# Performance work log

Hardware: AMD Instinct MI355X
Metric: run time of the kernel (lower is better)

## Reference

```python
import jax, jax.numpy as jnp
import numpy as np

EPS = 1e-6
NUM_SPECIAL = 4
NUM_HEADS = 16


def _rms_norm(x, w, eps=EPS):
    # x: [..., d], normalize over last dim
    var = jnp.mean(jnp.square(x), axis=-1, keepdims=True)
    return x * jax.lax.rsqrt(var + eps) * w


def _rotate_half(x):
    d = x.shape[-1] // 2
    return jnp.concatenate([-x[..., d:], x[..., :d]], axis=-1)


def _apply_rotary(q, k, cos, sin):
    # q,k: [B,H,N,hd]; cos,sin: [N,hd] -> broadcast [1,1,N,hd]
    cos = cos[None, None, :, :]
    sin = sin[None, None, :, :]
    q_out = q * cos + _rotate_half(q) * sin
    k_out = k * cos + _rotate_half(k) * sin
    return q_out, k_out


def _make_2d_mask(seq_len, num_special, window):
    # special tokens attend / are attended fully; patches use 2D local box
    patch_len = seq_len - num_special
    gs = int(round(patch_len ** 0.5))
    idx = jnp.arange(seq_len)
    special = idx < num_special
    p = idx - num_special
    row = p // gs
    col = p % gs
    special_case = special[:, None] | special[None, :]
    swa = (jnp.abs(row[:, None] - row[None, :]) <= window) & (
        jnp.abs(col[:, None] - col[None, :]) <= window)
    return special_case | swa  # [N, N] bool


def setup_inputs() -> dict:
    key = jax.random.key(0)
    ks = jax.random.split(key, 7)
    B, N, C = 4, 1028, 1024
    hd = C // NUM_HEADS
    return {
        "hidden_states": jax.random.normal(ks[0], (B, N, C), dtype=jnp.float32),
        "cos": jax.random.uniform(ks[1], (N, hd), dtype=jnp.float32),
        "sin": jax.random.uniform(ks[2], (N, hd), dtype=jnp.float32),
        "qkv_w": jax.random.normal(ks[3], (3 * C, C), dtype=jnp.float32) * (C ** -0.5),
        "out_w": jax.random.normal(ks[4], (C, C), dtype=jnp.float32) * (C ** -0.5),
        "norm_q_w": jnp.ones((hd,), dtype=jnp.float32),
        "norm_k_w": jnp.ones((hd,), dtype=jnp.float32),
        "sliding_window": 2,
    }


def reference(hidden_states, cos, sin, qkv_w, out_w, norm_q_w, norm_k_w, sliding_window):
    B, N, C = hidden_states.shape
    H = NUM_HEADS
    hd = C // H

    # fused QKV projection (nn.Linear: x @ W^T)
    qkv = jnp.einsum('bnc,dc->bnd', hidden_states, qkv_w)
    qkv = qkv.reshape(B, N, 3, H, hd).transpose(2, 0, 3, 1, 4)  # [3,B,H,N,hd]
    q, k, v = qkv[0], qkv[1], qkv[2]

    # per-head-dim RMSNorm on q and k
    q = _rms_norm(q, norm_q_w)
    k = _rms_norm(k, norm_k_w)

    # RoPE
    q, k = _apply_rotary(q, k, cos, sin)

    # 2D sliding-window + special-token mask
    mask = _make_2d_mask(N, NUM_SPECIAL, sliding_window)  # [N,N]

    scale = 1.0 / jnp.sqrt(jnp.asarray(hd, dtype=q.dtype))
    scores = jnp.einsum('bhqd,bhkd->bhqk', q, k) * scale
    neg = jnp.asarray(jnp.finfo(scores.dtype).min, dtype=scores.dtype)
    scores = jnp.where(mask[None, None, :, :], scores, neg)
    probs = jax.nn.softmax(scores, axis=-1)
    attn = jnp.einsum('bhqk,bhkd->bhqd', probs, v)  # [B,H,N,hd]

    attn = attn.transpose(0, 2, 1, 3).reshape(B, N, C)
    return jnp.einsum('bnc,dc->bnd', attn, out_w)
```

## Files before the change

kernel.cpp:

```cpp
#include <hip/hip_runtime.h>
#include <hip/hip_bf16.h>
#include <stdint.h>

typedef __bf16 bf16;
typedef __attribute__((ext_vector_type(8))) __bf16 bf16x8;
typedef __attribute__((ext_vector_type(4))) __bf16 bf16x4;
typedef __attribute__((ext_vector_type(4))) float f32x4;

#define NSEQ 1028
#define CDIM 1024
#define NHEADS 16
#define HD 64
#define BHN 64
#define NPAD 1088
#define M_REAL 4112
#define MTILES 33

static __device__ __forceinline__ void async_copy16(bf16* lds, const bf16* g) {
  __builtin_amdgcn_global_load_lds(
      (const __attribute__((address_space(1))) uint32_t*)g,
      (__attribute__((address_space(3))) uint32_t*)lds, 16, 0, 0);
}

__global__ __launch_bounds__(256) void cast_pad_kernel(const float* __restrict__ src,
                                                       bf16* __restrict__ dst,
                                                       long n_src, long n_dst) {
  long t = (long)blockIdx.x * 256 + threadIdx.x;
  long stride = (long)gridDim.x * 256;
  for (long j = t * 4; j < n_dst; j += stride * 4) {
    bf16x4 o;
    if (j + 4 <= n_src) {
      float4 v = *(const float4*)(src + j);
      o[0] = (bf16)v.x; o[1] = (bf16)v.y; o[2] = (bf16)v.z; o[3] = (bf16)v.w;
    } else {
      for (int k = 0; k < 4; k++) o[k] = (bf16)((j + k < n_src) ? src[j + k] : 0.0f);
    }
    *(bf16x4*)(dst + j) = o;
  }
}

template <int EPI, int NSTRIP>
__global__ __launch_bounds__(256) void gemm_bf16_kernel(
    const bf16* __restrict__ A, const bf16* __restrict__ Bm,
    bf16* __restrict__ q_bf, bf16* __restrict__ k_bf, bf16* __restrict__ v_raw,
    float* __restrict__ outF,
    const float* __restrict__ cosb, const float* __restrict__ sinb,
    const float* __restrict__ nqw, const float* __restrict__ nkw) {
  constexpr int K = CDIM;
  constexpr int N = NSTRIP * 8 * 128;
  __shared__ __attribute__((aligned(16))) bf16 As[2][128 * 64];
  __shared__ __attribute__((aligned(16))) bf16 Bs[2][128 * 64];
  const int tid = threadIdx.x;
  const int lane = tid & 63;
  const int wid = tid >> 6;
  const int wr = wid >> 1, wc = wid & 1;
  const int l15 = lane & 15, l4 = lane >> 4;

  const int xcd = blockIdx.x & 7;
  const int pos = blockIdx.x >> 3;
  const int nloc = pos % NSTRIP;
  const int mi = pos / NSTRIP;
  const int n0 = (xcd * NSTRIP + nloc) << 7;
  const int m0 = (mi < MTILES - 1) ? (mi << 7) : (M_REAL - 128);

  f32x4 acc[4][4] = {};

  size_t a_base[4], b_base[4];
#pragma unroll
  for (int s = 0; s < 4; s++) {
    int c = tid + s * 256;
    int row = c >> 3, ch = c & 7;
    int chs = ch ^ (row & 7);
    a_base[s] = (size_t)(m0 + row) * K + (chs << 3);
    b_base[s] = (size_t)(n0 + row) * K + (chs << 3);
  }

#define STAGE(bufi, ktof)                                         \
  {                                                               \
    _Pragma("unroll")                                             \
    for (int s = 0; s < 4; s++) {                                 \
      int c = tid + s * 256;                                      \
      async_copy16(&As[bufi][c * 8], A + a_base[s] + (ktof));     \
      async_copy16(&Bs[bufi][c * 8], Bm + b_base[s] + (ktof));    \
    }                                                             \
  }

  const int nt = K >> 6;
  STAGE(0, 0);

  for (int t = 0; t < nt; ++t) {
    if (t + 1 < nt) {
      STAGE((t + 1) & 1, (t + 1) << 6);
      asm volatile("s_waitcnt vmcnt(8)" ::: "memory");
    } else {
      asm volatile("s_waitcnt vmcnt(0)" ::: "memory");
    }
    __builtin_amdgcn_s_barrier();

    const int rsw = l15 & 7;
    const int cur = t & 1;
    bf16x8 af[2][4], bfr[2][4];
#pragma unroll
    for (int h = 0; h < 2; h++)
#pragma unroll
      for (int i = 0; i < 4; i++)
        af[h][i] = *(const bf16x8*)&As[cur][(wr * 64 + i * 16 + l15) * 64 +
                                            (((h * 4 + l4) ^ rsw) << 3)];
#pragma unroll
    for (int h = 0; h < 2; h++)
#pragma unroll
      for (int j = 0; j < 4; j++)
        bfr[h][j] = *(const bf16x8*)&Bs[cur][(wc * 64 + j * 16 + l15) * 64 +
                                             (((h * 4 + l4) ^ rsw) << 3)];

#pragma unroll
    for (int h = 0; h < 2; h++)
#pragma unroll
      for (int i = 0; i < 4; i++)
#pragma unroll
        for (int j = 0; j < 4; j++)
          acc[i][j] = __builtin_amdgcn_mfma_f32_16x16x32_bf16(af[h][i], bfr[h][j], acc[i][j], 0, 0, 0);

    asm volatile("s_waitcnt lgkmcnt(0)" ::: "memory");
    __builtin_amdgcn_s_barrier();
  }
#undef STAGE

  if (EPI == 0) {
    const int d_base = n0 + wc * 64;
    const int tsel = d_base >> 10;
    const int hh = (d_base & 1023) >> 6;
    if (tsel == 2) {
#pragma unroll
      for (int i = 0; i < 4; i++)
#pragma unroll
        for (int r = 0; r < 4; r++) {
          int m = m0 + wr * 64 + i * 16 + l4 * 4 + r;
          int b = m / NSEQ, n = m % NSEQ;
          size_t rb = ((size_t)(b * NHEADS + hh) * NSEQ + n) * HD;
#pragma unroll
          for (int j = 0; j < 4; j++)
            v_raw[rb + j * 16 + l15] = (bf16)acc[i][j][r];
        }
    } else {
      const float* wn = (tsel == 0) ? nqw : nkw;
      bf16* dst = (tsel == 0) ? q_bf : k_bf;
      float wv[4];
#pragma unroll
      for (int j = 0; j < 4; j++) wv[j] = wn[j * 16 + l15];
#pragma unroll
      for (int i = 0; i < 4; i++)
#pragma unroll
        for (int r = 0; r < 4; r++) {
          int m = m0 + wr * 64 + i * 16 + l4 * 4 + r;
          float ss = 0.0f;
#pragma unroll
          for (int j = 0; j < 4; j++) { float x = acc[i][j][r]; ss += x * x; }
          ss += __shfl_xor(ss, 1);
          ss += __shfl_xor(ss, 2);
          ss += __shfl_xor(ss, 4);
          ss += __shfl_xor(ss, 8);
          float rms = rsqrtf(ss * (1.0f / HD) + 1e-6f);
          int b = m / NSEQ, n = m % NSEQ;
          float qn[4];
#pragma unroll
          for (int j = 0; j < 4; j++) qn[j] = acc[i][j][r] * rms * wv[j];
          size_t rb = ((size_t)(b * NHEADS + hh) * NPAD + n) * HD;
#pragma unroll
          for (int j = 0; j < 4; j++) {
            float c = cosb[n * HD + j * 16 + l15];
            float s = sinb[n * HD + j * 16 + l15];
            float rot = (j < 2) ? -qn[j + 2] : qn[j - 2];
            dst[rb + j * 16 + l15] = (bf16)(qn[j] * c + rot * s);
          }
        }
    }
  } else {
#pragma unroll
    for (int i = 0; i < 4; i++)
#pragma unroll
      for (int j = 0; j < 4; j++) {
        int d = n0 + wc * 64 + j * 16 + l15;
        int mrow = m0 + wr * 64 + i * 16 + l4 * 4;
#pragma unroll
        for (int r = 0; r < 4; r++) {
          int m = mrow + r;
          outF[(size_t)m * N + d] = acc[i][j][r];
        }
      }
  }
}

__global__ __launch_bounds__(256) void v_transpose_kernel(const bf16* __restrict__ v_raw,
                                                          bf16* __restrict__ vT) {
  __shared__ bf16 tile[64][65];
  int bh = blockIdx.y, c = blockIdx.x;
  int tid = threadIdx.x;
#pragma unroll
  for (int jj = 0; jj < 16; jj++) {
    int idx = tid + jj * 256;
    int i = idx >> 6, e = idx & 63;
    int n = (c == 0) ? i : (64 * c - 60 + i);
    bool ok = (c == 0) ? (i < 4) : (n < NSEQ);
    tile[i][e] = ok ? v_raw[((size_t)bh * NSEQ + n) * HD + e] : (bf16)0.0f;
  }
  __syncthreads();
#pragma unroll
  for (int jj = 0; jj < 16; jj++) {
    int idx = tid + jj * 256;
    int e = idx >> 6, i = idx & 63;
    vT[((size_t)bh * HD + e) * NPAD + 64 * c + i] = tile[i][e];
  }
}

__global__ __launch_bounds__(256) void attn_kernel(
    const bf16* __restrict__ Q, const bf16* __restrict__ Kb, const bf16* __restrict__ Vt,
    bf16* __restrict__ att, const int* __restrict__ winp) {
  __shared__ __attribute__((aligned(16))) bf16 P_s[4][16][72];
  __shared__ float o_s[4][4][64];
  __shared__ float ml_s[4][2][16];
  const int bh = blockIdx.y, qt = blockIdx.x;
  const int W = winp[0];
  const int tid = threadIdx.x, w = tid >> 6, lane = tid & 63;
  const int l15 = lane & 15, l4 = lane >> 4;
  const size_t qkbase = (size_t)bh * NPAD * HD;
  const size_t vtb = (size_t)bh * HD * NPAD;
  const bool is_spec = (qt == 16);

  const int qrow0 = is_spec ? 0 : (4 + qt * 64 + w * 16);
  bf16x8 aq0 = *(const bf16x8*)&Q[qkbase + (size_t)(qrow0 + l15) * HD + l4 * 8];
  bf16x8 aq1 = *(const bf16x8*)&Q[qkbase + (size_t)(qrow0 + l15) * HD + 32 + l4 * 8];

  float mrow[4], lrow[4];
  f32x4 o[4] = {};
#pragma unroll
  for (int r = 0; r < 4; r++) { mrow[r] = -1e30f; lrow[r] = 0.0f; }

  int p0, pstep, pmax, toff;
  if (is_spec) {
    p0 = w; pstep = 4; pmax = 16; toff = -1;
  } else {
    int ta = ((2 * qt - W + 64) >> 1) - 32;
    int tb = (2 * qt + 1 + W) >> 1;
    ta = ta < 0 ? 0 : ta;
    tb = tb > 15 ? 15 : tb;
    p0 = 0; pstep = 1; pmax = tb - ta + 1; toff = ta - 1;
  }

  for (int p = p0; p <= pmax; p += pstep) {
    const bool sp = (p == 0);
    const int tau = toff + p;
    const int krow0 = sp ? 0 : (4 + tau * 64);
    const int vcol0 = sp ? 0 : (64 + tau * 64);

    f32x4 sacc[4] = {};
#pragma unroll
    for (int kf = 0; kf < 4; kf++) {
      const bf16* kp = &Kb[qkbase + (size_t)(krow0 + kf * 16 + l15) * HD];
      bf16x8 b0 = *(const bf16x8*)(kp + l4 * 8);
      bf16x8 b1 = *(const bf16x8*)(kp + 32 + l4 * 8);
      sacc[kf] = __builtin_amdgcn_mfma_f32_16x16x32_bf16(aq0, b0, sacc[kf], 0, 0, 0);
      sacc[kf] = __builtin_amdgcn_mfma_f32_16x16x32_bf16(aq1, b1, sacc[kf], 0, 0, 0);
    }

    float pvv[4][4];
#pragma unroll
    for (int kf = 0; kf < 4; kf++)
#pragma unroll
      for (int r = 0; r < 4; r++) {
        float s = sacc[kf][r] * 0.125f;
        bool valid;
        if (sp) {
          valid = (kf == 0) && (l15 < 4);
        } else if (is_spec) {
          valid = true;
        } else {
          int p_k = tau * 64 + kf * 16 + l15;
          int p_q = qt * 64 + w * 16 + l4 * 4 + r;
          int dr = (p_q >> 5) - (p_k >> 5); dr = dr < 0 ? -dr : dr;
          int dc = (p_q & 31) - (p_k & 31); dc = dc < 0 ? -dc : dc;
          valid = (dr <= W) && (dc <= W);
        }
        pvv[kf][r] = valid ? s : -1e30f;
      }

#pragma unroll
    for (int r = 0; r < 4; r++) {
      float mx = fmaxf(fmaxf(pvv[0][r], pvv[1][r]), fmaxf(pvv[2][r], pvv[3][r]));
#pragma unroll
      for (int mm = 1; mm < 16; mm <<= 1) mx = fmaxf(mx, __shfl_xor(mx, mm));
      float mnew = fmaxf(mrow[r], mx);
      float scale = __expf(mrow[r] - mnew);
      float rs = 0.0f;
#pragma unroll
      for (int kf = 0; kf < 4; kf++) {
        float pp = __expf(pvv[kf][r] - mnew);
        pvv[kf][r] = pp;
        rs += pp;
      }
#pragma unroll
      for (int mm = 1; mm < 16; mm <<= 1) rs += __shfl_xor(rs, mm);
      lrow[r] = lrow[r] * scale + rs;
      mrow[r] = mnew;
#pragma unroll
      for (int f = 0; f < 4; f++) o[f][r] *= scale;
    }

#pragma unroll
    for (int kf = 0; kf < 4; kf++)
#pragma unroll
      for (int r = 0; r < 4; r++)
        P_s[w][l4 * 4 + r][kf * 16 + l15] = (bf16)pvv[kf][r];

    bf16x8 pa0 = *(const bf16x8*)&P_s[w][l15][l4 * 8];
    bf16x8 pa1 = *(const bf16x8*)&P_s[w][l15][32 + l4 * 8];
#pragma unroll
    for (int f = 0; f < 4; f++) {
      const bf16* vp = &Vt[vtb + (size_t)(f * 16 + l15) * NPAD + vcol0];
      bf16x8 v0 = *(const bf16x8*)(vp + l4 * 8);
      bf16x8 v1 = *(const bf16x8*)(vp + 32 + l4 * 8);
      o[f] = __builtin_amdgcn_mfma_f32_16x16x32_bf16(pa0, v0, o[f], 0, 0, 0);
      o[f] = __builtin_amdgcn_mfma_f32_16x16x32_bf16(pa1, v1, o[f], 0, 0, 0);
    }
  }

  const int b = bh >> 4, h = bh & 15;
  if (!is_spec) {
#pragma unroll
    for (int f = 0; f < 4; f++)
#pragma unroll
      for (int r = 0; r < 4; r++) {
        int n = qrow0 + l4 * 4 + r;
        att[((size_t)(b * NSEQ + n)) * CDIM + h * HD + f * 16 + l15] =
            (bf16)(o[f][r] / lrow[r]);
      }
  } else {
    if (l4 == 0) {
#pragma unroll
      for (int f = 0; f < 4; f++)
#pragma unroll
        for (int r = 0; r < 4; r++) o_s[w][r][f * 16 + l15] = o[f][r];
      if (l15 == 0)
#pragma unroll
        for (int r = 0; r < 4; r++) { ml_s[w][0][r] = mrow[r]; ml_s[w][1][r] = lrow[r]; }
    }
    __syncthreads();
    int row = tid >> 6, dim = tid & 63;
    float M = -1e30f;
#pragma unroll
    for (int ww = 0; ww < 4; ww++) M = fmaxf(M, ml_s[ww][0][row]);
    float L = 0.0f, val = 0.0f;
#pragma unroll
    for (int ww = 0; ww < 4; ww++) {
      float e = __expf(ml_s[ww][0][row] - M);
      L += e * ml_s[ww][1][row];
      val += e * o_s[ww][row][dim];
    }
    att[((size_t)(b * NSEQ + row)) * CDIM + h * HD + dim] = (bf16)(val / L);
  }
}

extern "C" void kernel_launch(void* const* d_in, const int* in_sizes, int n_in,
                              void* d_out, int out_size, void* d_ws, size_t ws_size,
                              hipStream_t stream) {
  const float* hidden = (const float*)d_in[0];
  const float* cosb = (const float*)d_in[1];
  const float* sinb = (const float*)d_in[2];
  const float* qkv_w = (const float*)d_in[3];
  const float* out_w = (const float*)d_in[4];
  const float* norm_q_w = (const float*)d_in[5];
  const float* norm_k_w = (const float*)d_in[6];
  const int* win = (const int*)d_in[7];
  float* out = (float*)d_out;

  char* ws = (char*)d_ws;
  size_t off = 0;
  auto alloc = [&](size_t bytes) {
    char* p = ws + off;
    off += (bytes + 255) & ~(size_t)255;
    return p;
  };
  bf16* A_bf  = (bf16*)alloc((size_t)M_REAL * CDIM * 2);
  bf16* W1    = (bf16*)alloc((size_t)3 * CDIM * CDIM * 2);
  bf16* W2    = (bf16*)alloc((size_t)CDIM * CDIM * 2);
  bf16* v_raw = (bf16*)alloc((size_t)BHN * NSEQ * HD * 2);
  bf16* q_bf  = (bf16*)alloc((size_t)BHN * NPAD * HD * 2);
  bf16* k_bf  = (bf16*)alloc((size_t)BHN * NPAD * HD * 2);
  bf16* vT    = (bf16*)alloc((size_t)BHN * HD * NPAD * 2);
  bf16* att   = (bf16*)alloc((size_t)M_REAL * CDIM * 2);
  (void)ws_size; (void)in_sizes; (void)n_in; (void)out_size;

  cast_pad_kernel<<<2048, 256, 0, stream>>>(hidden, A_bf, (long)M_REAL * CDIM, (long)M_REAL * CDIM);
  cast_pad_kernel<<<1024, 256, 0, stream>>>(qkv_w, W1, (long)3 * CDIM * CDIM, (long)3 * CDIM * CDIM);
  cast_pad_kernel<<<512, 256, 0, stream>>>(out_w, W2, (long)CDIM * CDIM, (long)CDIM * CDIM);

  gemm_bf16_kernel<0, 3><<<792, 256, 0, stream>>>(
      A_bf, W1, q_bf, k_bf, v_raw, nullptr, cosb, sinb, norm_q_w, norm_k_w);
  v_transpose_kernel<<<dim3(17, 64), 256, 0, stream>>>(v_raw, vT);
  attn_kernel<<<dim3(17, 64), 256, 0, stream>>>(q_bf, k_bf, vT, att, win);
  gemm_bf16_kernel<1, 1><<<264, 256, 0, stream>>>(
      att, W2, nullptr, nullptr, nullptr, out, nullptr, nullptr, nullptr, nullptr);
}
```

Baseline: 136.8 us.

## Fuse three cast launches and halve GEMM K-tile for higher occupancy

Merges the three fp32-to-bf16 cast kernels into one launch that walks a concatenated index space, removing two kernel launches and their tail effects. The GEMM K-step shrinks from 64 to 32, which halves LDS per block (to 32 KB). A new swizzle scheme fits the 4-chunk rows, and launch_bounds now requests 4 blocks per CU for more occupancy. The cost is twice as many barrier-synchronized iterations, with less MFMA work per barrier to hide global-load latency.

```diff
diff --git a/kernel.cpp b/kernel.cpp
--- a/kernel.cpp
+++ b/kernel.cpp
@@ -22,25 +22,27 @@
       (__attribute__((address_space(3))) uint32_t*)lds, 16, 0, 0);
 }
 
-__global__ __launch_bounds__(256) void cast_pad_kernel(const float* __restrict__ src,
-                                                       bf16* __restrict__ dst,
-                                                       long n_src, long n_dst) {
+__global__ __launch_bounds__(256) void cast3_kernel(
+    const float* __restrict__ s0, bf16* __restrict__ d0, long n0,
+    const float* __restrict__ s1, bf16* __restrict__ d1, long n1,
+    const float* __restrict__ s2, bf16* __restrict__ d2, long n2) {
+  long total = n0 + n1 + n2;
   long t = (long)blockIdx.x * 256 + threadIdx.x;
   long stride = (long)gridDim.x * 256;
-  for (long j = t * 4; j < n_dst; j += stride * 4) {
+  for (long j = t * 4; j < total; j += stride * 4) {
+    const float* s; bf16* d; long jj = j;
+    if (jj < n0) { s = s0; d = d0; }
+    else if (jj < n0 + n1) { s = s1; d = d1; jj -= n0; }
+    else { s = s2; d = d2; jj -= n0 + n1; }
+    float4 v = *(const float4*)(s + jj);
     bf16x4 o;
-    if (j + 4 <= n_src) {
-      float4 v = *(const float4*)(src + j);
-      o[0] = (bf16)v.x; o[1] = (bf16)v.y; o[2] = (bf16)v.z; o[3] = (bf16)v.w;
-    } else {
-      for (int k = 0; k < 4; k++) o[k] = (bf16)((j + k < n_src) ? src[j + k] : 0.0f);
-    }
-    *(bf16x4*)(dst + j) = o;
+    o[0] = (bf16)v.x; o[1] = (bf16)v.y; o[2] = (bf16)v.z; o[3] = (bf16)v.w;
+    *(bf16x4*)(d + jj) = o;
   }
 }
 
 template <int EPI, int NSTRIP>
-__global__ __launch_bounds__(256) void gemm_bf16_kernel(
+__global__ __launch_bounds__(256, 4) void gemm_bf16_kernel(
     const bf16* __restrict__ A, const bf16* __restrict__ Bm,
     bf16* __restrict__ q_bf, bf16* __restrict__ k_bf, bf16* __restrict__ v_raw,
     float* __restrict__ outF,
@@ -48,8 +50,8 @@
     const float* __restrict__ nqw, const float* __restrict__ nkw) {
   constexpr int K = CDIM;
   constexpr int N = NSTRIP * 8 * 128;
-  __shared__ __attribute__((aligned(16))) bf16 As[2][128 * 64];
-  __shared__ __attribute__((aligned(16))) bf16 Bs[2][128 * 64];
+  __shared__ __attribute__((aligned(16))) bf16 As[2][128 * 32];
+  __shared__ __attribute__((aligned(16))) bf16 Bs[2][128 * 32];
   const int tid = threadIdx.x;
   const int lane = tid & 63;
   const int wid = tid >> 6;
@@ -65,61 +67,56 @@
 
   f32x4 acc[4][4] = {};
 
-  size_t a_base[4], b_base[4];
-#pragma unroll
-  for (int s = 0; s < 4; s++) {
+  size_t a_base[2], b_base[2];
+#pragma unroll
+  for (int s = 0; s < 2; s++) {
     int c = tid + s * 256;
-    int row = c >> 3, ch = c & 7;
-    int chs = ch ^ (row & 7);
-    a_base[s] = (size_t)(m0 + row) * K + (chs << 3);
-    b_base[s] = (size_t)(n0 + row) * K + (chs << 3);
+    int u = c ^ ((c >> 3) & 7);
+    int row = u >> 2, ch = u & 3;
+    a_base[s] = (size_t)(m0 + row) * K + (ch << 3);
+    b_base[s] = (size_t)(n0 + row) * K + (ch << 3);
   }
 
 #define STAGE(bufi, ktof)                                         \
   {                                                               \
     _Pragma("unroll")                                             \
-    for (int s = 0; s < 4; s++) {                                 \
+    for (int s = 0; s < 2; s++) {                                 \
       int c = tid + s * 256;                                      \
       async_copy16(&As[bufi][c * 8], A + a_base[s] + (ktof));     \
       async_copy16(&Bs[bufi][c * 8], Bm + b_base[s] + (ktof));    \
     }                                                             \
   }
 
-  const int nt = K >> 6;
+  const int nt = K >> 5;
   STAGE(0, 0);
 
   for (int t = 0; t < nt; ++t) {
     if (t + 1 < nt) {
-      STAGE((t + 1) & 1, (t + 1) << 6);
-      asm volatile("s_waitcnt vmcnt(8)" ::: "memory");
+      STAGE((t + 1) & 1, (t + 1) << 5);
+      asm volatile("s_waitcnt vmcnt(4)" ::: "memory");
     } else {
       asm volatile("s_waitcnt vmcnt(0)" ::: "memory");
     }
     __builtin_amdgcn_s_barrier();
 
-    const int rsw = l15 & 7;
     const int cur = t & 1;
-    bf16x8 af[2][4], bfr[2][4];
-#pragma unroll
-    for (int h = 0; h < 2; h++)
-#pragma unroll
-      for (int i = 0; i < 4; i++)
-        af[h][i] = *(const bf16x8*)&As[cur][(wr * 64 + i * 16 + l15) * 64 +
-                                            (((h * 4 + l4) ^ rsw) << 3)];
-#pragma unroll
-    for (int h = 0; h < 2; h++)
+    bf16x8 af[4], bfr[4];
+#pragma unroll
+    for (int i = 0; i < 4; i++) {
+      int u = ((wr * 64 + i * 16 + l15) << 2) | l4;
+      af[i] = *(const bf16x8*)&As[cur][(u ^ ((u >> 3) & 7)) << 3];
+    }
+#pragma unroll
+    for (int j = 0; j < 4; j++) {
+      int u = ((wc * 64 + j * 16 + l15) << 2) | l4;
+      bfr[j] = *(const bf16x8*)&Bs[cur][(u ^ ((u >> 3) & 7)) << 3];
+    }
+
+#pragma unroll
+    for (int i = 0; i < 4; i++)
 #pragma unroll
       for (int j = 0; j < 4; j++)
-        bfr[h][j] = *(const bf16x8*)&Bs[cur][(wc * 64 + j * 16 + l15) * 64 +
-                                             (((h * 4 + l4) ^ rsw) << 3)];
-
-#pragma unroll
-    for (int h = 0; h < 2; h++)
-#pragma unroll
-      for (int i = 0; i < 4; i++)
-#pragma unroll
-        for (int j = 0; j < 4; j++)
-          acc[i][j] = __builtin_amdgcn_mfma_f32_16x16x32_bf16(af[h][i], bfr[h][j], acc[i][j], 0, 0, 0);
+        acc[i][j] = __builtin_amdgcn_mfma_f32_16x16x32_bf16(af[i], bfr[j], acc[i][j], 0, 0, 0);
 
     asm volatile("s_waitcnt lgkmcnt(0)" ::: "memory");
     __builtin_amdgcn_s_barrier();
@@ -390,9 +387,10 @@
   bf16* att   = (bf16*)alloc((size_t)M_REAL * CDIM * 2);
   (void)ws_size; (void)in_sizes; (void)n_in; (void)out_size;
 
-  cast_pad_kernel<<<2048, 256, 0, stream>>>(hidden, A_bf, (long)M_REAL * CDIM, (long)M_REAL * CDIM);
-  cast_pad_kernel<<<1024, 256, 0, stream>>>(qkv_w, W1, (long)3 * CDIM * CDIM, (long)3 * CDIM * CDIM);
-  cast_pad_kernel<<<512, 256, 0, stream>>>(out_w, W2, (long)CDIM * CDIM, (long)CDIM * CDIM);
+  cast3_kernel<<<2048, 256, 0, stream>>>(
+      hidden, A_bf, (long)M_REAL * CDIM,
+      qkv_w, W1, (long)3 * CDIM * CDIM,
+      out_w, W2, (long)CDIM * CDIM);
 
   gemm_bf16_kernel<0, 3><<<792, 256, 0, stream>>>(
       A_bf, W1, q_bf, k_bf, v_raw, nullptr, cosb, sinb, norm_q_w, norm_k_w);
```

Result: faster. 130.6 us (-4.5%).
